# Kernel optimization log

Measured on AMD Instinct MI355X. Metric: run time of the kernel, lower is better.

The kernel has to match this reference:

```python
import jax, jax.numpy as jnp
import numpy as np

N_LEVELS = 16
F = 2
LOG2_3D = 15
LOG2_4D = 22
B_PTS = 262144
PRIMES = [1, 2654435761, 805459861, 3674653429]

# per-level resolutions: floor(base * b**i), b = exp((log(fin)-log(base))/(L-1))
_b = np.exp((np.log(512.0) - np.log(16.0)) / (N_LEVELS - 1))
_bt = np.exp((np.log(32.0) - np.log(2.0)) / (N_LEVELS - 1))
RES = np.floor(16.0 * _b ** np.arange(N_LEVELS)).astype(np.float32)
RES_T = np.floor(2.0 * _bt ** np.arange(N_LEVELS)).astype(np.float32)

# corner offsets; first coordinate is the outermost bit (matches torch interp ordering)
OFF3 = np.array([[i, j, k] for i in (0, 1) for j in (0, 1) for k in (0, 1)], dtype=np.int32)
OFF4 = np.array([[i, j, k, l] for i in (0, 1) for j in (0, 1) for k in (0, 1) for l in (0, 1)], dtype=np.int32)


def _hash(coords, log2_size):
    # coords: [..., D] int32 (non-negative). Low bits of (c_i * p_i) are wrap-invariant,
    # and the final mask keeps < 32 bits, so uint32 math matches torch's int64 hash.
    c = coords.astype(jnp.uint32)
    h = c[..., 0] * jnp.uint32(PRIMES[0] & 0xFFFFFFFF)
    for i in range(1, coords.shape[-1]):
        h = h ^ (c[..., i] * jnp.uint32(PRIMES[i] & 0xFFFFFFFF))
    return (h & jnp.uint32((1 << log2_size) - 1)).astype(jnp.int32)


def _level_embed(x, table, box_min, box_max, res_vec, log2_size, offsets):
    # x: [B, D]; table: [T, F]; res_vec: [D]; offsets: [2^D, D]
    grid = (box_max - box_min) / res_vec                       # [D] voxel size
    xc = jnp.clip(x, box_min, box_max)
    bl = jnp.floor((xc - box_min) / grid)                      # [B, D] bottom-left idx
    vmin = bl * grid + box_min                                 # voxel_min_vertex
    w = (x - vmin) / grid                                      # interp weights (uses unclamped x, as in torch)
    idx = bl.astype(jnp.int32)[:, None, :] + offsets[None]     # [B, 2^D, D]
    v = table[_hash(idx, log2_size)]                           # [B, 2^D, F] irregular gather
    D = x.shape[-1]
    for d in range(D):                                         # multilinear reduce, dim 0 outermost
        n = v.shape[1] // 2
        wd = w[:, d][:, None, None]
        v = v[:, :n] * (1 - wd) + v[:, n:] * wd
    return v[:, 0]                                             # [B, F]


def _multires_embed(x, tables, box_min, box_max, res_levels, log2_size, offsets):
    outs = [_level_embed(x, tables[i], box_min, box_max,
                         jnp.asarray(res_levels[i], dtype=jnp.float32),
                         log2_size, jnp.asarray(offsets))
            for i in range(N_LEVELS)]
    return jnp.concatenate(outs, axis=-1)                      # [B, L*F]


def _forward(x, emb4d, emb3d):
    bmin4 = jnp.zeros(4, jnp.float32)
    bmax4 = jnp.ones(4, jnp.float32)
    bmin3, bmax3 = bmin4[:3], bmax4[:3]
    res4 = np.stack([RES, RES, RES, RES_T], axis=1)            # [L, 4]
    res3 = np.stack([RES, RES, RES], axis=1)                   # [L, 3]
    e4 = _multires_embed(x, emb4d, bmin4, bmax4, res4, LOG2_4D, OFF4)
    e3 = _multires_embed(x[:, :3], emb3d, bmin3, bmax3, res3, LOG2_3D, OFF3)
    embedded = e4 + e3                                         # modus='add'
    keep4 = jnp.all((x >= bmin4) & (x <= bmax4), axis=-1)
    keep3 = jnp.all((x[:, :3] >= bmin3) & (x[:, :3] <= bmax3), axis=-1)
    return embedded, keep4 & keep3


def setup_inputs() -> dict:
    key = jax.random.key(0)
    k1, k2, k3 = jax.random.split(key, 3)
    x = jax.random.uniform(k1, (B_PTS, 4), dtype=jnp.float32)
    emb4d = jax.random.uniform(k2, (N_LEVELS, 2 ** LOG2_4D, F), dtype=jnp.float32,
                               minval=-1e-4, maxval=1e-4)
    emb3d = jax.random.uniform(k3, (N_LEVELS, 2 ** LOG2_3D, F), dtype=jnp.float32,
                               minval=-1e-4, maxval=1e-4)
    return {"x": x, "emb4d": emb4d, "emb3d": emb3d}


def reference(x, emb4d, emb3d):
    return _forward(x, emb4d, emb3d)
```

## Files before the change

kernel.cpp:

```cpp
#include <hip/hip_runtime.h>
#include <math.h>
#include <stdint.h>

#define B_PTS   262144
#define NLEV    16
#define MASK4   ((1u << 22) - 1u)
#define MASK3   ((1u << 15) - 1u)
#define P1      2654435761u
#define P2      805459861u
#define P3      3674653429u

#define LSH     4
#define NSHL    (NLEV - LSH)
#define NCHUNK  256

typedef float f32x4 __attribute__((ext_vector_type(4)));

struct LevelParams {
    float res[NLEV];
    float rest[NLEV];
};

struct PtState {
    uint32_t a;
    uint32_t t1e, t1o, t2e, t2o, t3e, t3o;
    float w0, w1, w2, w3;
};

__device__ __forceinline__ PtState mk_fast(float xx, float xy, float xz, float xw,
                                           float R, float Rt)
{
    PtState st;
    const float xd[4] = { xx, xy, xz, xw };
    const float rv[4] = { R, R, R, Rt };
    uint32_t tt[4][2]; float ww[4];
    #pragma unroll
    for (int d = 0; d < 4; ++d) {
        float xc = fminf(fmaxf(xd[d], 0.0f), 1.0f);
        float bl = floorf(xc * rv[d]);
        float w  = fmaf(xd[d], rv[d], -bl);
        uint32_t bi = (uint32_t)(int)bl;
        uint32_t prime = (d == 0) ? 1u : (d == 1) ? P1 : (d == 2) ? P2 : P3;
        tt[d][0] = bi * prime;
        tt[d][1] = tt[d][0] + prime;
        ww[d] = w;
    }
    st.a   = tt[0][0];
    st.t1e = tt[1][0]; st.t1o = tt[1][1];
    st.t2e = tt[2][0]; st.t2o = tt[2][1];
    st.t3e = tt[3][0]; st.t3o = tt[3][1];
    st.w0 = ww[0]; st.w1 = ww[1]; st.w2 = ww[2]; st.w3 = ww[3];
    return st;
}

__device__ __forceinline__ uint32_t bfr(float v) {
    uint32_t u = __float_as_uint(v);
    u += 0x7FFFu + ((u >> 16) & 1u);
    return u >> 16;
}

__global__ __launch_bounds__(256)
void k_shard(const float4* __restrict__ x,
             const float2* __restrict__ emb4d,
             uint32_t* __restrict__ ws2, LevelParams lp)
{
    const int bid   = blockIdx.x;
    const int s     = bid & 7;
    const int rest  = bid >> 3;
    const int chunk = rest & (NCHUNK - 1);
    const int levi  = rest >> 8;
    const int lev   = LSH + levi;
    const uint32_t sh = (uint32_t)s;

    const float2* tab4 = emb4d + ((size_t)lev << 22);
    const float R = lp.res[lev], Rt = lp.rest[lev];
    const int pbase = chunk * 1024 + threadIdx.x;
    uint32_t* dst = ws2 + (size_t)(levi * 8 + s) * B_PTS + pbase;

    #pragma unroll
    for (int i = 0; i < 4; ++i) {
        f32x4 xr = __builtin_nontemporal_load(
            reinterpret_cast<const f32x4*>(&x[pbase + i * 256]));
        PtState st = mk_fast(xr.x, xr.y, xr.z, xr.w, R, Rt);

        const float w1e = 1.0f - st.w1, w2e = 1.0f - st.w2, w3e = 1.0f - st.w3;
        const float q00 = w1e * w2e, q01 = w1e * st.w2,
                    q10 = st.w1 * w2e, q11 = st.w1 * st.w2;
        const float wc[8] = { q00 * w3e, q00 * st.w3, q01 * w3e, q01 * st.w3,
                              q10 * w3e, q10 * st.w3, q11 * w3e, q11 * st.w3 };
        const float wx0 = 1.0f - st.w0, wx1 = st.w0;
        const uint32_t a0 = st.a, a1 = a0 + 1u;
        const bool odd = (a0 & 1u) != 0u;

        float4   q[8];
        float2   e2[8];
        uint32_t hib = 0;

        #pragma unroll
        for (int pp = 0; pp < 8; ++pp) {
            uint32_t E = (((pp & 4) ? st.t1o : st.t1e) ^
                          ((pp & 2) ? st.t2o : st.t2e) ^
                          ((pp & 1) ? st.t3o : st.t3e)) & MASK4;
            uint32_t h0 = E ^ a0;
            hib |= (h0 & 1u) << pp;
            float4 qq = make_float4(0.0f, 0.0f, 0.0f, 0.0f);
            float2 ee = make_float2(0.0f, 0.0f);
            const bool act = (E >> 19) == sh;
            if (act)
                qq = *reinterpret_cast<const float4*>(tab4 + (h0 & ~1u));
            if (act && odd)
                ee = tab4[E ^ a1];
            q[pp] = qq; e2[pp] = ee;
        }

        float ex = 0.0f, ey = 0.0f;
        #pragma unroll
        for (int pp = 0; pp < 8; ++pp) {
            const bool hi = (hib >> pp) & 1u;
            float c0x = hi ? q[pp].z : q[pp].x;
            float c0y = hi ? q[pp].w : q[pp].y;
            float c1x = odd ? e2[pp].x : (hi ? q[pp].x : q[pp].z);
            float c1y = odd ? e2[pp].y : (hi ? q[pp].y : q[pp].w);
            float u0 = wc[pp] * wx0, u1 = wc[pp] * wx1;
            ex = fmaf(c0x, u0, fmaf(c1x, u1, ex));
            ey = fmaf(c0y, u0, fmaf(c1y, u1, ey));
        }

        uint32_t pk = bfr(ex) | (bfr(ey) << 16);
        __builtin_nontemporal_store(pk, dst + i * 256);
    }
}

__global__ __launch_bounds__(256)
void k_final(const float4* __restrict__ x,
             const float2* __restrict__ emb4d,
             const float2* __restrict__ emb3d,
             const uint32_t* __restrict__ ws2,
             float* __restrict__ out, float* __restrict__ keep,
             LevelParams lp)
{
    __shared__ float tile[256 * 9];
    const int t    = threadIdx.x;
    const int p    = blockIdx.x * 256 + t;
    const int lev0 = blockIdx.y * 4;

    const float4 xv = x[p];

    #pragma unroll
    for (int l4 = 0; l4 < 4; ++l4) {
        const int lev = lev0 + l4;
        PtState st = mk_fast(xv.x, xv.y, xv.z, xv.w, lp.res[lev], lp.rest[lev]);
        const uint32_t a0 = st.a, a1 = st.a + 1u;
        const bool odd = (a0 & 1u) != 0u;
        const float wx0 = 1.0f - st.w0, wx1 = st.w0;
        const float wy[2] = { 1.0f - st.w1, st.w1 };
        const float wz[2] = { 1.0f - st.w2, st.w2 };
        const float wwv[2] = { 1.0f - st.w3, st.w3 };

        float ex = 0.0f, ey = 0.0f;

        if (lev >= LSH) {
            const int li = lev - LSH;
            #pragma unroll
            for (int s2 = 0; s2 < 8; ++s2) {
                uint32_t w = ws2[(size_t)(li * 8 + s2) * B_PTS + p];
                ex += __uint_as_float(w << 16);
                ey += __uint_as_float(w & 0xFFFF0000u);
            }
        }

        {
            const float2* tab3 = emb3d + ((size_t)lev << 15);
            #pragma unroll
            for (int pp = 0; pp < 4; ++pp) {
                uint32_t E = (((pp & 2) ? st.t1o : st.t1e) ^
                              ((pp & 1) ? st.t2o : st.t2e)) & MASK3;
                uint32_t h0 = E ^ a0;
                float4 qq = *reinterpret_cast<const float4*>(tab3 + (h0 & ~1u));
                float2 ee = make_float2(0.0f, 0.0f);
                if (odd) ee = tab3[E ^ a1];
                const bool hi = (h0 & 1u) != 0u;
                float c0x = hi ? qq.z : qq.x, c0y = hi ? qq.w : qq.y;
                float c1x = odd ? ee.x : (hi ? qq.x : qq.z);
                float c1y = odd ? ee.y : (hi ? qq.y : qq.w);
                float wp = wy[(pp >> 1) & 1] * wz[pp & 1];
                ex = fmaf(c0x, wp * wx0, fmaf(c1x, wp * wx1, ex));
                ey = fmaf(c0y, wp * wx0, fmaf(c1y, wp * wx1, ey));
            }
        }

        if (lev < LSH) {
            const float2* tab4 = emb4d + ((size_t)lev << 22);
            #pragma unroll
            for (int pp = 0; pp < 8; ++pp) {
                uint32_t E = (((pp & 4) ? st.t1o : st.t1e) ^
                              ((pp & 2) ? st.t2o : st.t2e) ^
                              ((pp & 1) ? st.t3o : st.t3e)) & MASK4;
                uint32_t h0 = E ^ a0;
                float4 qq = *reinterpret_cast<const float4*>(tab4 + (h0 & ~1u));
                float2 ee = make_float2(0.0f, 0.0f);
                if (odd) ee = tab4[E ^ a1];
                const bool hi = (h0 & 1u) != 0u;
                float c0x = hi ? qq.z : qq.x, c0y = hi ? qq.w : qq.y;
                float c1x = odd ? ee.x : (hi ? qq.x : qq.z);
                float c1y = odd ? ee.y : (hi ? qq.y : qq.w);
                float wp = wy[(pp >> 2) & 1] * wz[(pp >> 1) & 1] * wwv[pp & 1];
                ex = fmaf(c0x, wp * wx0, fmaf(c1x, wp * wx1, ex));
                ey = fmaf(c0y, wp * wx0, fmaf(c1y, wp * wx1, ey));
            }
        }

        tile[t * 9 + 2 * l4]     = ex;
        tile[t * 9 + 2 * l4 + 1] = ey;
    }

    __syncthreads();

    float* ob = out + (size_t)blockIdx.x * (256 * 32) + lev0 * 2;
    #pragma unroll
    for (int k = 0; k < 8; ++k) {
        int idx = k * 256 + t;
        int row = idx >> 3, col = idx & 7;
        ob[(size_t)row * 32 + col] = tile[row * 9 + col];
    }

    if (blockIdx.y == 0) {
        bool k4 = (xv.x >= 0.0f) && (xv.x <= 1.0f) &&
                  (xv.y >= 0.0f) && (xv.y <= 1.0f) &&
                  (xv.z >= 0.0f) && (xv.z <= 1.0f) &&
                  (xv.w >= 0.0f) && (xv.w <= 1.0f);
        keep[p] = k4 ? 1.0f : 0.0f;
    }
}

__global__ __launch_bounds__(256)
void embed_all(const float4* __restrict__ x,
               const float2* __restrict__ emb4d,
               const float2* __restrict__ emb3d,
               float* __restrict__ out,
               float* __restrict__ keep,
               LevelParams lp)
{
    __shared__ float tile[16 * 33];
    const int t = threadIdx.x;
    const int pl = t & 15;
    const int lev = t >> 4;
    const int pbase = blockIdx.x * 16;

    const float4 xv = x[pbase + pl];
    PtState st = mk_fast(xv.x, xv.y, xv.z, xv.w, lp.res[lev], lp.rest[lev]);
    const uint32_t a0 = st.a, a1 = st.a + 1u;
    const float wx[2] = { 1.0f - st.w0, st.w0 };
    const float wy[2] = { 1.0f - st.w1, st.w1 };
    const float wz[2] = { 1.0f - st.w2, st.w2 };
    const float wwv[2] = { 1.0f - st.w3, st.w3 };
    float ex = 0.0f, ey = 0.0f;

    const float2* tab4 = emb4d + ((size_t)lev << 22);
    #pragma unroll
    for (int c = 0; c < 16; ++c) {
        uint32_t E = ((c & 4) ? st.t1o : st.t1e) ^ ((c & 2) ? st.t2o : st.t2e) ^
                     ((c & 1) ? st.t3o : st.t3e);
        uint32_t h = (E ^ ((c & 8) ? a1 : a0)) & MASK4;
        float wt = wx[(c >> 3) & 1] * wy[(c >> 2) & 1] *
                   wz[(c >> 1) & 1] * wwv[c & 1];
        float2 v = tab4[h];
        ex = fmaf(v.x, wt, ex);
        ey = fmaf(v.y, wt, ey);
    }
    const float2* tab3 = emb3d + ((size_t)lev << 15);
    #pragma unroll
    for (int c = 0; c < 8; ++c) {
        uint32_t E = ((c & 2) ? st.t1o : st.t1e) ^ ((c & 1) ? st.t2o : st.t2e);
        uint32_t h = (E ^ ((c & 4) ? a1 : a0)) & MASK3;
        float wt = wx[(c >> 2) & 1] * wy[(c >> 1) & 1] * wz[c & 1];
        float2 v = tab3[h];
        ex = fmaf(v.x, wt, ex);
        ey = fmaf(v.y, wt, ey);
    }

    tile[pl * 33 + 2 * lev]     = ex;
    tile[pl * 33 + 2 * lev + 1] = ey;
    __syncthreads();
    {
        int pw = t >> 4;
        int cw = (2 * t) & 31;
        float2 v = make_float2(tile[pw * 33 + cw], tile[pw * 33 + cw + 1]);
        *reinterpret_cast<float2*>(out + (size_t)pbase * 32 + 2 * t) = v;
    }
    if (t < 16) {
        const float4 xk = x[pbase + t];
        bool k4 = (xk.x >= 0.0f) && (xk.x <= 1.0f) &&
                  (xk.y >= 0.0f) && (xk.y <= 1.0f) &&
                  (xk.z >= 0.0f) && (xk.z <= 1.0f) &&
                  (xk.w >= 0.0f) && (xk.w <= 1.0f);
        keep[pbase + t] = k4 ? 1.0f : 0.0f;
    }
}

extern "C" void kernel_launch(void* const* d_in, const int* in_sizes, int n_in,
                              void* d_out, int out_size, void* d_ws, size_t ws_size,
                              hipStream_t stream)
{
    const float4* x     = (const float4*)d_in[0];
    const float2* emb4d = (const float2*)d_in[1];
    const float2* emb3d = (const float2*)d_in[2];
    float* out  = (float*)d_out;
    float* keep = out + (size_t)B_PTS * 32;

    LevelParams lp;
    const double b  = exp((log(512.0) - log(16.0)) / 15.0);
    const double bt = exp((log(32.0)  - log(2.0))  / 15.0);
    for (int i = 0; i < NLEV; ++i) {
        lp.res[i]  = (float)floor(16.0 * pow(b,  (double)i));
        lp.rest[i] = (float)floor(2.0  * pow(bt, (double)i));
    }

    const size_t ws2_bytes = (size_t)NSHL * 8 * B_PTS * 4;

    if (ws_size >= ws2_bytes && d_ws != nullptr) {
        uint32_t* ws2 = (uint32_t*)d_ws;
        k_shard<<<NSHL * NCHUNK * 8,    256, 0, stream>>>(x, emb4d, ws2, lp);
        k_final<<<dim3(B_PTS / 256, 4), 256, 0, stream>>>(x, emb4d, emb3d,
                                                          ws2, out, keep, lp);
    } else {
        embed_all<<<B_PTS / 16, 256, 0, stream>>>(x, emb4d, emb3d, out, keep, lp);
    }
}
```

Measured before the change: 477.6 us.

## Software-pipeline sharded hash gathers with inline asm loads and explicit vmcnt waits

```diff
diff --git a/kernel.cpp b/kernel.cpp
--- a/kernel.cpp
+++ b/kernel.cpp
@@ -59,7 +59,59 @@
     return u >> 16;
 }
 
-__global__ __launch_bounds__(256)
+struct Gather {
+    float2 v[16];
+    float  wc[8];
+    float  wx0, wx1;
+};
+
+__device__ __forceinline__ void issue_g(const float2* __restrict__ tab4,
+                                        const PtState& st, uint32_t sh,
+                                        Gather& g)
+{
+    const float w1e = 1.0f - st.w1, w2e = 1.0f - st.w2, w3e = 1.0f - st.w3;
+    const float q00 = w1e * w2e, q01 = w1e * st.w2,
+                q10 = st.w1 * w2e, q11 = st.w1 * st.w2;
+    const float wcv[8] = { q00 * w3e, q00 * st.w3, q01 * w3e, q01 * st.w3,
+                           q10 * w3e, q10 * st.w3, q11 * w3e, q11 * st.w3 };
+    g.wx0 = 1.0f - st.w0; g.wx1 = st.w0;
+    const uint32_t a0 = st.a, a1 = a0 + 1u;
+    const uint32_t dummy_off = (sh << 19) * 8u;
+
+    #pragma unroll
+    for (int pp = 0; pp < 8; ++pp) {
+        uint32_t E = (((pp & 4) ? st.t1o : st.t1e) ^
+                      ((pp & 2) ? st.t2o : st.t2e) ^
+                      ((pp & 1) ? st.t3o : st.t3e)) & MASK4;
+        const bool act = (E >> 19) == sh;
+        uint32_t off0 = act ? (E ^ a0) * 8u : dummy_off;
+        uint32_t off1 = act ? (E ^ a1) * 8u : dummy_off;
+        asm volatile("global_load_dwordx2 %0, %1, %2"
+                     : "=v"(g.v[2 * pp]) : "v"(off0), "s"(tab4));
+        asm volatile("global_load_dwordx2 %0, %1, %2"
+                     : "=v"(g.v[2 * pp + 1]) : "v"(off1), "s"(tab4));
+        g.wc[pp] = act ? wcv[pp] : 0.0f;
+    }
+}
+
+__device__ __forceinline__ uint32_t consume_g(const Gather& g)
+{
+    float ex = 0.0f, ey = 0.0f;
+    #pragma unroll
+    for (int pp = 0; pp < 8; ++pp) {
+        float u0 = g.wc[pp] * g.wx0, u1 = g.wc[pp] * g.wx1;
+        ex = fmaf(g.v[2 * pp].x, u0, fmaf(g.v[2 * pp + 1].x, u1, ex));
+        ey = fmaf(g.v[2 * pp].y, u0, fmaf(g.v[2 * pp + 1].y, u1, ey));
+    }
+    return bfr(ex) | (bfr(ey) << 16);
+}
+
+#define VMWAIT(N) do {                                            \
+    asm volatile("s_waitcnt vmcnt(" #N ")" ::: "memory");         \
+    __builtin_amdgcn_sched_barrier(0);                            \
+} while (0)
+
+__global__ __launch_bounds__(256, 2)
 void k_shard(const float4* __restrict__ x,
              const float2* __restrict__ emb4d,
              uint32_t* __restrict__ ws2, LevelParams lp)
@@ -77,58 +129,37 @@
     const int pbase = chunk * 1024 + threadIdx.x;
     uint32_t* dst = ws2 + (size_t)(levi * 8 + s) * B_PTS + pbase;
 
-    #pragma unroll
-    for (int i = 0; i < 4; ++i) {
-        f32x4 xr = __builtin_nontemporal_load(
-            reinterpret_cast<const f32x4*>(&x[pbase + i * 256]));
-        PtState st = mk_fast(xr.x, xr.y, xr.z, xr.w, R, Rt);
-
-        const float w1e = 1.0f - st.w1, w2e = 1.0f - st.w2, w3e = 1.0f - st.w3;
-        const float q00 = w1e * w2e, q01 = w1e * st.w2,
-                    q10 = st.w1 * w2e, q11 = st.w1 * st.w2;
-        const float wc[8] = { q00 * w3e, q00 * st.w3, q01 * w3e, q01 * st.w3,
-                              q10 * w3e, q10 * st.w3, q11 * w3e, q11 * st.w3 };
-        const float wx0 = 1.0f - st.w0, wx1 = st.w0;
-        const uint32_t a0 = st.a, a1 = a0 + 1u;
-        const bool odd = (a0 & 1u) != 0u;
-
-        float4   q[8];
-        float2   e2[8];
-        uint32_t hib = 0;
-
-        #pragma unroll
-        for (int pp = 0; pp < 8; ++pp) {
-            uint32_t E = (((pp & 4) ? st.t1o : st.t1e) ^
-                          ((pp & 2) ? st.t2o : st.t2e) ^
-                          ((pp & 1) ? st.t3o : st.t3e)) & MASK4;
-            uint32_t h0 = E ^ a0;
-            hib |= (h0 & 1u) << pp;
-            float4 qq = make_float4(0.0f, 0.0f, 0.0f, 0.0f);
-            float2 ee = make_float2(0.0f, 0.0f);
-            const bool act = (E >> 19) == sh;
-            if (act)
-                qq = *reinterpret_cast<const float4*>(tab4 + (h0 & ~1u));
-            if (act && odd)
-                ee = tab4[E ^ a1];
-            q[pp] = qq; e2[pp] = ee;
-        }
-
-        float ex = 0.0f, ey = 0.0f;
-        #pragma unroll
-        for (int pp = 0; pp < 8; ++pp) {
-            const bool hi = (hib >> pp) & 1u;
-            float c0x = hi ? q[pp].z : q[pp].x;
-            float c0y = hi ? q[pp].w : q[pp].y;
-            float c1x = odd ? e2[pp].x : (hi ? q[pp].x : q[pp].z);
-            float c1y = odd ? e2[pp].y : (hi ? q[pp].y : q[pp].w);
-            float u0 = wc[pp] * wx0, u1 = wc[pp] * wx1;
-            ex = fmaf(c0x, u0, fmaf(c1x, u1, ex));
-            ey = fmaf(c0y, u0, fmaf(c1y, u1, ey));
-        }
-
-        uint32_t pk = bfr(ex) | (bfr(ey) << 16);
-        __builtin_nontemporal_store(pk, dst + i * 256);
-    }
+    f32x4 x0 = *reinterpret_cast<const f32x4*>(&x[pbase]);
+    f32x4 x1 = *reinterpret_cast<const f32x4*>(&x[pbase + 256]);
+    f32x4 x2 = *reinterpret_cast<const f32x4*>(&x[pbase + 512]);
+    f32x4 x3 = *reinterpret_cast<const f32x4*>(&x[pbase + 768]);
+    asm volatile("" : "+v"(x0), "+v"(x1), "+v"(x2), "+v"(x3));
+    asm volatile("s_waitcnt vmcnt(0)" ::: "memory");
+
+    Gather A, B;
+    PtState st;
+
+    st = mk_fast(x0.x, x0.y, x0.z, x0.w, R, Rt);
+    issue_g(tab4, st, sh, A);
+    st = mk_fast(x1.x, x1.y, x1.z, x1.w, R, Rt);
+    issue_g(tab4, st, sh, B);
+    VMWAIT(16);
+    uint32_t pk0 = consume_g(A);
+    st = mk_fast(x2.x, x2.y, x2.z, x2.w, R, Rt);
+    issue_g(tab4, st, sh, A);
+    VMWAIT(16);
+    uint32_t pk1 = consume_g(B);
+    st = mk_fast(x3.x, x3.y, x3.z, x3.w, R, Rt);
+    issue_g(tab4, st, sh, B);
+    VMWAIT(16);
+    uint32_t pk2 = consume_g(A);
+    VMWAIT(0);
+    uint32_t pk3 = consume_g(B);
+
+    __builtin_nontemporal_store(pk0, dst);
+    __builtin_nontemporal_store(pk1, dst + 256);
+    __builtin_nontemporal_store(pk2, dst + 512);
+    __builtin_nontemporal_store(pk3, dst + 768);
 }
 
 __global__ __launch_bounds__(256)
```

Measured after the change: 438.6 us (median of 7 runs). -8.2%, faster.
